# Optimization experiments

Measured on AMD Instinct MI355X. Metric: run time of the kernel, lower is better.

The kernel has to match this reference:

```python
import jax, jax.numpy as jnp
import numpy as np

N_NODES = 100000
N_EDGES = 1600000
IN_DIM = 128
HID = 128
OUT_DIM = 64
EPS = 1e-8


def setup_inputs() -> dict:
    key = jax.random.key(0)
    ks = jax.random.split(key, 10)
    x = jax.random.normal(ks[0], (N_NODES, IN_DIM), dtype=jnp.float32)
    edge_index = jax.random.randint(ks[1], (2, N_EDGES), 0, N_NODES, dtype=jnp.int64)
    edge_attr = jax.random.uniform(ks[2], (N_EDGES, 4), dtype=jnp.float32)
    s1 = 1.0 / np.sqrt(IN_DIM)
    s2 = 1.0 / np.sqrt(HID)
    sr = 1.0 / np.sqrt(2 * HID)
    W1 = jax.random.normal(ks[3], (HID, IN_DIM), dtype=jnp.float32) * s1
    b1 = jnp.zeros((HID,), dtype=jnp.float32)
    W2 = jax.random.normal(ks[4], (HID, HID), dtype=jnp.float32) * s2
    b2 = jnp.zeros((HID,), dtype=jnp.float32)
    Wr = jax.random.normal(ks[5], (OUT_DIM, 2 * HID), dtype=jnp.float32) * sr
    br = jnp.zeros((OUT_DIM,), dtype=jnp.float32)
    return {"x": x, "edge_index": edge_index, "edge_attr": edge_attr,
            "W1": W1, "b1": b1, "W2": W2, "b2": b2, "Wr": Wr, "br": br}


def _edge_weight_from_attr_auto(edge_attr):
    # mean over features, min-max normalize, invert, clamp >= 0
    m = edge_attr.mean(axis=-1)                      # [E]
    m_min, m_max = m.min(), m.max()
    m_norm = (m - m_min) / (m_max - m_min + EPS)
    w = jnp.where(m_max - m_min > EPS, 1.0 - m_norm, jnp.ones_like(m))
    return jnp.clip(w, 0.0)


def reference(x, edge_index, edge_attr, W1, b1, W2, b2, Wr, br):
    N = x.shape[0]
    row, col = edge_index[0], edge_index[1]          # source -> target
    ew = _edge_weight_from_attr_auto(edge_attr)      # [E]
    # GCN normalization with self-loops (self-loop weight = 1.0)
    deg = jax.ops.segment_sum(ew, col, num_segments=N) + 1.0   # [N]
    dis = jax.lax.rsqrt(deg)                         # deg >= 1
    norm = dis[row] * ew * dis[col]                  # [E]

    def gcn(h, W, b):
        hW = h @ W.T                                 # [N, d_out]
        agg = jax.ops.segment_sum(norm[:, None] * hW[row], col, num_segments=N)
        # self-loop contribution: dis[i] * 1.0 * dis[i] * hW[i]
        return agg + (dis * dis)[:, None] * hW + b

    # dropout in eval mode -> identity
    h1 = jax.nn.relu(gcn(x, W1, b1))                 # [N, HID]
    h2 = jax.nn.relu(gcn(h1, W2, b2))                # [N, HID]
    hcat = jnp.concatenate([h1, h2], axis=-1)        # [N, 2*HID] (JK concat)
    return hcat @ Wr.T + br                          # residue-level [N, OUT_DIM]
```

## Files before the change

kernel.cpp:

```cpp
#include <hip/hip_runtime.h>

#define NN 100000
#define NE 1600000
#define HID 128
#define ODIM 64
#define NBK 196
#define BSHIFT 9
#define BGRID 512
#define CVTB 48
#define CHUNK 3125
#define BITER 13
#define BINCAP 12288
#define SMAX 4504
#define LMAX 568

typedef unsigned int u32;
typedef unsigned short u16;
typedef __bf16 bf16x8 __attribute__((ext_vector_type(8)));
typedef float f32x4 __attribute__((ext_vector_type(4)));
typedef float f32x2 __attribute__((ext_vector_type(2)));

__device__ __forceinline__ float bf_lo(u32 p){ return __uint_as_float(p << 16); }
__device__ __forceinline__ float bf_hi(u32 p){ return __uint_as_float(p & 0xffff0000u); }
__device__ __forceinline__ u16 f2bf(float f){
  u32 u = __float_as_uint(f);
  u += 0x7fffu + ((u >> 16) & 1u);
  return (u16)(u >> 16);
}
__device__ __forceinline__ bf16x8 ld8bf(const u16* p){ return *(const bf16x8*)p; }
__device__ __forceinline__ bf16x8 cvt8(const float* p){
  union { bf16x8 v; u16 s[8]; } r;
#pragma unroll
  for (int i = 0; i < 8; i++) r.s[i] = f2bf(p[i]);
  return r.v;
}

__global__ __launch_bounds__(256) void k_bin(
    const float* __restrict__ eattr, const int* __restrict__ erow,
    const int* __restrict__ ecol, u32* __restrict__ bcur,
    uint2* __restrict__ bin, u32* __restrict__ minmax, u32* __restrict__ cnt,
    const float* __restrict__ W1, const float* __restrict__ W2,
    const float* __restrict__ Wr, u16* __restrict__ W1b,
    u16* __restrict__ W2b, u16* __restrict__ Wrb){
  int tid = threadIdx.x;
  if (blockIdx.x >= BGRID){
    int i = (blockIdx.x - BGRID) * 256 + tid;
    const float* src; u16* dst; int off;
    if (i < 4096){ src = W1; dst = W1b; off = i; }
    else if (i < 8192){ src = W2; dst = W2b; off = i - 4096; }
    else { src = Wr; dst = Wrb; off = i - 8192; }
    float4 v = ((const float4*)src)[off];
    uint2 o;
    o.x = (u32)f2bf(v.x) | ((u32)f2bf(v.y) << 16);
    o.y = (u32)f2bf(v.z) | ((u32)f2bf(v.w) << 16);
    ((uint2*)dst)[off] = o;
    return;
  }
  __shared__ u32 lcnt4[4 * NBK], wof4[4 * NBK];
  __shared__ u32 lofs[NBK], gb[NBK];
  __shared__ u32 scn[256];
  __shared__ u16 lmap[LMAX];
  __shared__ uint2 stage[SMAX];
  __shared__ u32 Tt;
  __shared__ float smin[4], smax[4];
  for (int t = tid; t < 4 * NBK; t += 256) lcnt4[t] = 0;
  __syncthreads();
  int base = blockIdx.x * CHUNK;
  int wid = tid >> 6, lane = tid & 63;
  float lmin = __uint_as_float(0x7f800000u), lmax = 0.f;
  u32 pk[BITER]; float mv[BITER]; u32 sv[BITER];
#pragma unroll
  for (int it = 0; it < BITER; it++){
    int idx = it * 256 + tid;
    u32 p = 0xFFFFFFFFu; float m = 0.f; u32 s = 0;
    if (idx < CHUNK){
      int e = base + idx;
      float4 a = ((const float4*)eattr)[e];
      m = 0.25f * (a.x + a.y + a.z + a.w);
      lmin = fminf(lmin, m); lmax = fmaxf(lmax, m);
      int c = ecol[e];
      s = (u32)erow[e]; if (s >= NN) s = 0;
      if ((u32)c < NN){
        u32 b = (u32)c >> BSHIFT;
        u32 r = atomicAdd(&lcnt4[wid * NBK + b], 1u);
        p = (b << 21) | (((u32)c & 511u) << 12) | r;
        atomicAdd(&cnt[c], 1u);
      }
    }
    pk[it] = p; mv[it] = m; sv[it] = s;
  }
  __syncthreads();
  u32 na = 0, n = 0;
  if (tid < NBK){
    u32 n0 = lcnt4[tid], n1 = lcnt4[NBK + tid];
    u32 n2 = lcnt4[2 * NBK + tid], n3 = lcnt4[3 * NBK + tid];
    n = n0 + n1 + n2 + n3;
    na = (n + 7u) & ~7u;
    wof4[tid] = 0; wof4[NBK + tid] = n0;
    wof4[2 * NBK + tid] = n0 + n1; wof4[3 * NBK + tid] = n0 + n1 + n2;
  }
  scn[tid] = na; __syncthreads();
  for (int s = 1; s < 256; s <<= 1){
    u32 t = (tid >= s) ? scn[tid - s] : 0;
    __syncthreads();
    scn[tid] += t;
    __syncthreads();
  }
  u32 ex = scn[tid] - na;
  if (tid < NBK){
    lofs[tid] = ex;
    u32 g = 0x80000000u;
    if (na){
      u32 gl = atomicAdd(&bcur[tid], na);
      if (gl + na <= BINCAP) g = (u32)tid * BINCAP + gl;
    }
    gb[tid] = g;
    for (u32 l = ex >> 3; l < (ex + na) >> 3; l++) lmap[l] = (u16)tid;
    uint2 sent; sent.x = 0xFFFFFFFFu; sent.y = 0u;
    for (u32 k = n; k < na; k++) stage[ex + k] = sent;
  }
  if (tid == 255) Tt = scn[255];
  __syncthreads();
#pragma unroll
  for (int it = 0; it < BITER; it++){
    u32 p = pk[it];
    if (p == 0xFFFFFFFFu) continue;
    u32 b = p >> 21;
    uint2 rec; rec.x = sv[it] | (((p >> 12) & 511u) << 17); rec.y = __float_as_uint(mv[it]);
    stage[lofs[b] + wof4[wid * NBK + b] + (p & 4095u)] = rec;
  }
  __syncthreads();
  u32 T = Tt;
  for (u32 i = tid; i < T; i += 256){
    u32 b = lmap[i >> 3];
    u32 g = gb[b];
    if (g != 0x80000000u) bin[g + (i - lofs[b])] = stage[i];
  }
  for (int off = 32; off; off >>= 1){
    lmin = fminf(lmin, __shfl_xor(lmin, off));
    lmax = fmaxf(lmax, __shfl_xor(lmax, off));
  }
  if (lane == 0){ smin[wid] = lmin; smax[wid] = lmax; }
  __syncthreads();
  if (tid == 0){
    float mn = fminf(fminf(smin[0], smin[1]), fminf(smin[2], smin[3]));
    float mx = fmaxf(fmaxf(smax[0], smax[1]), fmaxf(smax[2], smax[3]));
    atomicMax(&minmax[0], ~__float_as_uint(mn));
    atomicMax(&minmax[1], __float_as_uint(mx));
  }
}

__global__ __launch_bounds__(512) void k_scan(
    const u32* __restrict__ cnt, u32* __restrict__ meta, u32* __restrict__ cur){
  __shared__ u32 wtot[8];
  int b = blockIdx.x, tid = threadIdx.x;
  int wid = tid >> 6, lane = tid & 63;
  int node = (b << BSHIFT) + tid;
  u32 v = (node < NN) ? cnt[node] : 0u;
  u32 incl = v;
  for (int off = 1; off < 64; off <<= 1){
    u32 t = (u32)__shfl_up((int)incl, off);
    if (lane >= off) incl += t;
  }
  if (lane == 63) wtot[wid] = incl;
  __syncthreads();
  u32 pre = 0;
#pragma unroll
  for (int k = 0; k < 8; k++) pre += (k < wid) ? wtot[k] : 0u;
  u32 rs = (u32)(b * BINCAP) + pre + incl - v;
  if (node < NN){
    meta[node] = rs | (v << 22);
    cur[node] = rs;
  }
}

__global__ __launch_bounds__(1024) void k_scatter(
    const u32* __restrict__ bcur, const uint2* __restrict__ bin,
    const u32* __restrict__ minmax, const u32* __restrict__ cur,
    u32* __restrict__ csr, float* __restrict__ dis){
  __shared__ u32 curL[512], degL[512];
  int b = blockIdx.x, tid = threadIdx.x;
  int bb = b * BINCAP;
  int nrec = (int)min(bcur[b], (u32)BINCAP);
  if (tid < 512){
    int node = (b << BSHIFT) + tid;
    curL[tid] = (node < NN) ? cur[node] : 0u;
    degL[tid] = 0u;
  }
  __syncthreads();
  float mn  = __uint_as_float(~minmax[0]);
  float mx  = __uint_as_float(minmax[1]);
  float rng = mx - mn;
  bool flat = !(rng > 1e-8f);
  float inv = 1.f / (rng + 1e-8f);
  for (int i = tid; i < nrec; i += 1024){
    uint2 r = bin[bb + i];
    if (r.x == 0xFFFFFFFFu) continue;
    u32 d = (r.x >> 17) & 511u;
    float w = flat ? 1.f : fmaxf(1.f - (__uint_as_float(r.y) - mn) * inv, 0.f);
    u32 pos = atomicAdd(&curL[d], 1u);
    csr[pos] = (r.x & 0x1FFFFu) | ((u32)(w * 32767.f + 0.5f) << 17);
    atomicAdd(&degL[d], (u32)(w * 1048576.f + 0.5f));
  }
  __syncthreads();
  if (tid < 512){
    int node = (b << BSHIFT) + tid;
    if (node < NN) dis[node] = rsqrtf(1.f + (float)degL[tid] * (1.f / 1048576.f));
  }
}

template <bool A_F32>
__global__ __launch_bounds__(256) void k_gemm128(
    const void* __restrict__ Av, const u16* __restrict__ Bt,
    const float* __restrict__ dis, u16* __restrict__ G){
  int wave = threadIdx.x >> 6, lane = threadIdx.x & 63;
  int m0 = blockIdx.x * 32;
  int m = lane & 15, q = lane >> 4;
  const float* a0f = (const float*)Av + (size_t)(m0 + m) * HID;
  const float* a1f = a0f + (size_t)16 * HID;
  const u16*   a0b = (const u16*)Av   + (size_t)(m0 + m) * HID;
  const u16*   a1b = a0b + (size_t)16 * HID;
  const u16* brow0 = Bt + (size_t)(wave * 16 + m) * HID;
  const u16* brow1 = brow0 + (size_t)64 * HID;
  f32x4 acc00 = {0.f,0.f,0.f,0.f}, acc01 = {0.f,0.f,0.f,0.f};
  f32x4 acc10 = {0.f,0.f,0.f,0.f}, acc11 = {0.f,0.f,0.f,0.f};
#pragma unroll
  for (int kb = 0; kb < HID; kb += 32){
    bf16x8 af0 = A_F32 ? cvt8(a0f + kb + q * 8) : ld8bf(a0b + kb + q * 8);
    bf16x8 af1 = A_F32 ? cvt8(a1f + kb + q * 8) : ld8bf(a1b + kb + q * 8);
    bf16x8 bf0 = ld8bf(brow0 + kb + q * 8);
    bf16x8 bf1 = ld8bf(brow1 + kb + q * 8);
    acc00 = __builtin_amdgcn_mfma_f32_16x16x32_bf16(af0, bf0, acc00, 0, 0, 0);
    acc01 = __builtin_amdgcn_mfma_f32_16x16x32_bf16(af0, bf1, acc01, 0, 0, 0);
    acc10 = __builtin_amdgcn_mfma_f32_16x16x32_bf16(af1, bf0, acc10, 0, 0, 0);
    acc11 = __builtin_amdgcn_mfma_f32_16x16x32_bf16(af1, bf1, acc11, 0, 0, 0);
  }
  u16* crow0 = G + (size_t)(m0 + q * 4) * HID + wave * 16 + m;
  u16* crow1 = crow0 + (size_t)16 * HID;
#pragma unroll
  for (int r = 0; r < 4; r++){
    float d0 = dis[m0 + q * 4 + r];
    float d1 = dis[m0 + 16 + q * 4 + r];
    crow0[(size_t)r * HID]      = f2bf(acc00[r] * d0);
    crow0[(size_t)r * HID + 64] = f2bf(acc01[r] * d0);
    crow1[(size_t)r * HID]      = f2bf(acc10[r] * d1);
    crow1[(size_t)r * HID + 64] = f2bf(acc11[r] * d1);
  }
}

__global__ __launch_bounds__(256) void k_aggregate(
    const u32* __restrict__ meta, const u32* __restrict__ csr,
    const float* __restrict__ dis, const u16* __restrict__ g,
    const float* __restrict__ bias, u16* __restrict__ hout){
  int node = __builtin_amdgcn_readfirstlane(
      (int)(blockIdx.x * 4 + (threadIdx.x >> 6)));
  int lane = threadIdx.x & 63;
  const u32* gp = (const u32*)g;
  u32 sv = gp[((size_t)node << 6) + lane];
  u32 mw = meta[node];
  float di = dis[node];
  u32 s = mw & 0x3FFFFFu;
  int c = (int)(mw >> 22);
  const u32* cp = csr + s;
  f32x2 acc = {0.f, 0.f};
  int j = 0;
  for (; j + 16 <= c; j += 16){
    u32 p[16];
#pragma unroll
    for (int t = 0; t < 16; t++)
      p[t] = __builtin_amdgcn_readfirstlane(cp[j + t]);
    u32 pv[16];
#pragma unroll
    for (int t = 0; t < 16; t++)
      pv[t] = gp[(size_t)(p[t] & 0x1FFFFu) * 64u + lane];
#pragma unroll
    for (int t = 0; t < 16; t++){
      float wf = (float)(p[t] >> 17);
      f32x2 val = {bf_lo(pv[t]), bf_hi(pv[t])};
      f32x2 w2 = {wf, wf};
      acc += w2 * val;
    }
  }
  for (; j < c; j += 8){
    u32 p[8];
#pragma unroll
    for (int t = 0; t < 8; t++)
      p[t] = __builtin_amdgcn_readfirstlane(cp[j + t]);
    u32 st[8]; u32 wi[8];
#pragma unroll
    for (int t = 0; t < 8; t++){
      bool ok = (j + t) < c;
      st[t] = ok ? (p[t] & 0x1FFFFu) : 0u;
      wi[t] = ok ? (p[t] >> 17) : 0u;
    }
    u32 pv[8];
#pragma unroll
    for (int t = 0; t < 8; t++)
      pv[t] = gp[(size_t)st[t] * 64u + lane];
#pragma unroll
    for (int t = 0; t < 8; t++){
      float wf = (float)wi[t];
      f32x2 val = {bf_lo(pv[t]), bf_hi(pv[t])};
      f32x2 w2 = {wf, wf};
      acc += w2 * val;
    }
  }
  float2 bv = ((const float2*)bias)[lane];
  f32x2 selfv = {bf_lo(sv), bf_hi(sv)};
  float d2 = di * (1.f / 32767.f);
  float o0 = fmaxf(acc.x * d2 + (selfv.x * di + bv.x), 0.f);
  float o1 = fmaxf(acc.y * d2 + (selfv.y * di + bv.y), 0.f);
  ((u32*)hout)[((size_t)node << 6) + lane] = (u32)f2bf(o0) | ((u32)f2bf(o1) << 16);
}

__global__ __launch_bounds__(256) void k_readout(
    const u16* __restrict__ h1, const u16* __restrict__ h2,
    const u16* __restrict__ Wrb, const float* __restrict__ br, float* __restrict__ out){
  int wave = threadIdx.x >> 6, lane = threadIdx.x & 63;
  int m0 = blockIdx.x * 32;
  int n0 = wave * 16;
  int m = lane & 15, q = lane >> 4;
  const u16* a10 = h1 + (size_t)(m0 + m) * HID;
  const u16* a11 = a10 + (size_t)16 * HID;
  const u16* a20 = h2 + (size_t)(m0 + m) * HID;
  const u16* a21 = a20 + (size_t)16 * HID;
  const u16* b  = Wrb + (size_t)(n0 + m) * (2 * HID);
  f32x4 acc0 = {0.f,0.f,0.f,0.f}, acc1 = {0.f,0.f,0.f,0.f};
#pragma unroll
  for (int kb = 0; kb < HID; kb += 32){
    bf16x8 bf = ld8bf(b + kb + q * 8);
    acc0 = __builtin_amdgcn_mfma_f32_16x16x32_bf16(ld8bf(a10 + kb + q * 8), bf, acc0, 0, 0, 0);
    acc1 = __builtin_amdgcn_mfma_f32_16x16x32_bf16(ld8bf(a11 + kb + q * 8), bf, acc1, 0, 0, 0);
  }
#pragma unroll
  for (int kb = 0; kb < HID; kb += 32){
    bf16x8 bf = ld8bf(b + HID + kb + q * 8);
    acc0 = __builtin_amdgcn_mfma_f32_16x16x32_bf16(ld8bf(a20 + kb + q * 8), bf, acc0, 0, 0, 0);
    acc1 = __builtin_amdgcn_mfma_f32_16x16x32_bf16(ld8bf(a21 + kb + q * 8), bf, acc1, 0, 0, 0);
  }
  float bias = br[n0 + m];
  float* crow0 = out + (size_t)(m0 + q * 4) * ODIM + n0 + m;
  float* crow1 = crow0 + (size_t)16 * ODIM;
#pragma unroll
  for (int r = 0; r < 4; r++){
    crow0[(size_t)r * ODIM] = acc0[r] + bias;
    crow1[(size_t)r * ODIM] = acc1[r] + bias;
  }
}

extern "C" void kernel_launch(void* const* d_in, const int* in_sizes, int n_in,
                              void* d_out, int out_size, void* d_ws, size_t ws_size,
                              hipStream_t stream){
  const float* x     = (const float*)d_in[0];
  const int*   eidx  = (const int*)d_in[1];
  const float* eattr = (const float*)d_in[2];
  const float* W1    = (const float*)d_in[3];
  const float* b1    = (const float*)d_in[4];
  const float* W2    = (const float*)d_in[5];
  const float* b2    = (const float*)d_in[6];
  const float* Wr    = (const float*)d_in[7];
  const float* br    = (const float*)d_in[8];
  const int* erow  = eidx;
  const int* ecol  = eidx + NE;

  char* w = (char*)d_ws;
  auto carve = [&](size_t bytes) -> void* {
    void* p = (void*)w;
    w += (bytes + 255) & ~(size_t)255;
    return p;
  };
  u32* csr       = (u32*)carve((size_t)NBK * BINCAP * 4);
  u32* bcur      = (u32*)carve(256 * 4);
  u32* minmax    = (u32*)carve(256);
  u32* cnt       = (u32*)carve((size_t)NN * 4);
  u32* cur       = (u32*)carve((size_t)NN * 4);
  u32* meta      = (u32*)carve((size_t)NN * 4);
  float* dis     = (float*)carve((size_t)NN * 4);
  u16* W1b       = (u16*)carve((size_t)HID * HID * 2);
  u16* W2b       = (u16*)carve((size_t)HID * HID * 2);
  u16* Wrb       = (u16*)carve((size_t)ODIM * 2 * HID * 2);
  u16* g         = (u16*)carve((size_t)NN * HID * 2);
  u16* h1        = (u16*)carve((size_t)NN * HID * 2);
  u16* h2        = (u16*)carve((size_t)NN * HID * 2);
  uint2* bin     = (uint2*)h2;

  size_t zspan = (size_t)((char*)cnt + (size_t)NN * 4 - (char*)bcur);
  hipMemsetAsync(bcur, 0, zspan, stream);
  k_bin<<<BGRID + CVTB, 256, 0, stream>>>(eattr, erow, ecol, bcur, bin, minmax,
                                          cnt, W1, W2, Wr, W1b, W2b, Wrb);
  k_scan<<<NBK, 512, 0, stream>>>(cnt, meta, cur);
  k_scatter<<<NBK, 1024, 0, stream>>>(bcur, bin, minmax, cur, csr, dis);

  k_gemm128<true><<<NN / 32, 256, 0, stream>>>(x, W1b, dis, g);
  k_aggregate<<<NN / 4, 256, 0, stream>>>(meta, csr, dis, g, b1, h1);
  k_gemm128<false><<<NN / 32, 256, 0, stream>>>(h1, W2b, dis, g);
  k_aggregate<<<NN / 4, 256, 0, stream>>>(meta, csr, dis, g, b2, h2);
  k_readout<<<NN / 32, 256, 0, stream>>>(h1, h2, Wrb, br, (float*)d_out);
}
```

Measured before the change: 429.0 us.

## Quantize edge means, defer min-max normalization, and fuse degree scan into scatter

Edge attribute means are quantized to 15-bit integers in the binning pass, so min/max become integer atomics and the edge weight becomes an affine function of the stored code, applied later. The global per-node count atomics and the separate scan kernel are removed. Counts, weight sums, the per-bin prefix scan and dis are now computed inside the scatter kernel from the binned records. The bin record shrinks from 8 to 6 bytes, split into u32 and u16 arrays, and the binning grid is enlarged with smaller chunks. The risk is quantizing the mean before normalization, which changes accuracy slightly. The scatter kernel also gains an extra pass over the bin.

```diff
diff --git a/kernel.cpp b/kernel.cpp
--- a/kernel.cpp
+++ b/kernel.cpp
@@ -6,13 +6,13 @@
 #define ODIM 64
 #define NBK 196
 #define BSHIFT 9
-#define BGRID 512
+#define BGRID 800
 #define CVTB 48
-#define CHUNK 3125
-#define BITER 13
+#define CHUNK 2000
+#define BITER 8
 #define BINCAP 12288
-#define SMAX 4504
-#define LMAX 568
+#define SMAX 2588
+#define LMAX 647
 
 typedef unsigned int u32;
 typedef unsigned short u16;
@@ -35,10 +35,19 @@
   return r.v;
 }
 
+__device__ __forceinline__ void wparams(const u32* minmax, float* A, float* B){
+  u32 mnq = 32767u - minmax[0];
+  u32 mxq = minmax[1];
+  u32 rngq = mxq - mnq;
+  float inv = rngq ? 1.f / ((float)rngq * (1.f / 32767.f) + 1e-8f) : 0.f;
+  *A = 1.f + (float)mnq * (1.f / 32767.f) * inv;
+  *B = inv * (1.f / 32767.f);
+}
+
 __global__ __launch_bounds__(256) void k_bin(
     const float* __restrict__ eattr, const int* __restrict__ erow,
     const int* __restrict__ ecol, u32* __restrict__ bcur,
-    uint2* __restrict__ bin, u32* __restrict__ minmax, u32* __restrict__ cnt,
+    u32* __restrict__ binA, u16* __restrict__ binM, u32* __restrict__ minmax,
     const float* __restrict__ W1, const float* __restrict__ W2,
     const float* __restrict__ Wr, u16* __restrict__ W1b,
     u16* __restrict__ W2b, u16* __restrict__ Wrb){
@@ -60,34 +69,36 @@
   __shared__ u32 lofs[NBK], gb[NBK];
   __shared__ u32 scn[256];
   __shared__ u16 lmap[LMAX];
-  __shared__ uint2 stage[SMAX];
+  __shared__ u32 stageA[SMAX];
+  __shared__ u16 stageM[SMAX];
   __shared__ u32 Tt;
-  __shared__ float smin[4], smax[4];
+  __shared__ u32 sMn[4], sMx[4];
   for (int t = tid; t < 4 * NBK; t += 256) lcnt4[t] = 0;
   __syncthreads();
   int base = blockIdx.x * CHUNK;
   int wid = tid >> 6, lane = tid & 63;
-  float lmin = __uint_as_float(0x7f800000u), lmax = 0.f;
-  u32 pk[BITER]; float mv[BITER]; u32 sv[BITER];
+  u32 lmn = 0, lmx = 0;
+  u32 pk[BITER], sd[BITER], mq8[BITER];
 #pragma unroll
   for (int it = 0; it < BITER; it++){
     int idx = it * 256 + tid;
-    u32 p = 0xFFFFFFFFu; float m = 0.f; u32 s = 0;
+    u32 p = 0xFFFFFFFFu, srcd = 0, mq = 0;
     if (idx < CHUNK){
       int e = base + idx;
       float4 a = ((const float4*)eattr)[e];
-      m = 0.25f * (a.x + a.y + a.z + a.w);
-      lmin = fminf(lmin, m); lmax = fmaxf(lmax, m);
+      float m = 0.25f * (a.x + a.y + a.z + a.w);
+      mq = (u32)(m * 32767.f + 0.5f);
+      lmn = max(lmn, 32767u - mq); lmx = max(lmx, mq);
       int c = ecol[e];
-      s = (u32)erow[e]; if (s >= NN) s = 0;
+      u32 s = (u32)erow[e]; if (s >= NN) s = 0;
       if ((u32)c < NN){
         u32 b = (u32)c >> BSHIFT;
         u32 r = atomicAdd(&lcnt4[wid * NBK + b], 1u);
-        p = (b << 21) | (((u32)c & 511u) << 12) | r;
-        atomicAdd(&cnt[c], 1u);
+        p = (b << 21) | r;
+        srcd = s | (((u32)c & 511u) << 17);
       }
     }
-    pk[it] = p; mv[it] = m; sv[it] = s;
+    pk[it] = p; sd[it] = srcd; mq8[it] = mq;
   }
   __syncthreads();
   u32 na = 0, n = 0;
@@ -95,7 +106,7 @@
     u32 n0 = lcnt4[tid], n1 = lcnt4[NBK + tid];
     u32 n2 = lcnt4[2 * NBK + tid], n3 = lcnt4[3 * NBK + tid];
     n = n0 + n1 + n2 + n3;
-    na = (n + 7u) & ~7u;
+    na = (n + 3u) & ~3u;
     wof4[tid] = 0; wof4[NBK + tid] = n0;
     wof4[2 * NBK + tid] = n0 + n1; wof4[3 * NBK + tid] = n0 + n1 + n2;
   }
@@ -115,9 +126,8 @@
       if (gl + na <= BINCAP) g = (u32)tid * BINCAP + gl;
     }
     gb[tid] = g;
-    for (u32 l = ex >> 3; l < (ex + na) >> 3; l++) lmap[l] = (u16)tid;
-    uint2 sent; sent.x = 0xFFFFFFFFu; sent.y = 0u;
-    for (u32 k = n; k < na; k++) stage[ex + k] = sent;
+    for (u32 l = ex >> 2; l < (ex + na) >> 2; l++) lmap[l] = (u16)tid;
+    for (u32 k = n; k < na; k++){ stageA[ex + k] = 0xFFFFFFFFu; stageM[ex + k] = 0; }
   }
   if (tid == 255) Tt = scn[255];
   __syncthreads();
@@ -126,86 +136,86 @@
     u32 p = pk[it];
     if (p == 0xFFFFFFFFu) continue;
     u32 b = p >> 21;
-    uint2 rec; rec.x = sv[it] | (((p >> 12) & 511u) << 17); rec.y = __float_as_uint(mv[it]);
-    stage[lofs[b] + wof4[wid * NBK + b] + (p & 4095u)] = rec;
+    u32 slot = lofs[b] + wof4[wid * NBK + b] + (p & 4095u);
+    stageA[slot] = sd[it];
+    stageM[slot] = (u16)mq8[it];
   }
   __syncthreads();
   u32 T = Tt;
   for (u32 i = tid; i < T; i += 256){
-    u32 b = lmap[i >> 3];
+    u32 b = lmap[i >> 2];
     u32 g = gb[b];
-    if (g != 0x80000000u) bin[g + (i - lofs[b])] = stage[i];
+    if (g != 0x80000000u){
+      u32 o = g + (i - lofs[b]);
+      binA[o] = stageA[i];
+      binM[o] = stageM[i];
+    }
   }
   for (int off = 32; off; off >>= 1){
-    lmin = fminf(lmin, __shfl_xor(lmin, off));
-    lmax = fmaxf(lmax, __shfl_xor(lmax, off));
-  }
-  if (lane == 0){ smin[wid] = lmin; smax[wid] = lmax; }
+    lmn = max(lmn, (u32)__shfl_xor((int)lmn, off));
+    lmx = max(lmx, (u32)__shfl_xor((int)lmx, off));
+  }
+  if (lane == 0){ sMn[wid] = lmn; sMx[wid] = lmx; }
   __syncthreads();
   if (tid == 0){
-    float mn = fminf(fminf(smin[0], smin[1]), fminf(smin[2], smin[3]));
-    float mx = fmaxf(fmaxf(smax[0], smax[1]), fmaxf(smax[2], smax[3]));
-    atomicMax(&minmax[0], ~__float_as_uint(mn));
-    atomicMax(&minmax[1], __float_as_uint(mx));
-  }
-}
-
-__global__ __launch_bounds__(512) void k_scan(
-    const u32* __restrict__ cnt, u32* __restrict__ meta, u32* __restrict__ cur){
+    u32 mn = max(max(sMn[0], sMn[1]), max(sMn[2], sMn[3]));
+    u32 mx = max(max(sMx[0], sMx[1]), max(sMx[2], sMx[3]));
+    atomicMax(&minmax[0], mn);
+    atomicMax(&minmax[1], mx);
+  }
+}
+
+__global__ __launch_bounds__(1024) void k_scatter(
+    const u32* __restrict__ bcur, const u32* __restrict__ binA,
+    const u16* __restrict__ binM, const u32* __restrict__ minmax,
+    u32* __restrict__ csr, u32* __restrict__ meta, float* __restrict__ dis){
+  __shared__ u32 cntL[512], sumL[512], curL[512];
   __shared__ u32 wtot[8];
   int b = blockIdx.x, tid = threadIdx.x;
+  int bb = b * BINCAP;
+  int nrec = (int)min(bcur[b], (u32)BINCAP);
+  if (tid < 512){ cntL[tid] = 0; sumL[tid] = 0; }
+  __syncthreads();
+  for (int i = tid; i < nrec; i += 1024){
+    u32 a = binA[bb + i];
+    if (a == 0xFFFFFFFFu) continue;
+    u32 d = (a >> 17) & 511u;
+    u32 mq = binM[bb + i];
+    atomicAdd(&cntL[d], 1u);
+    atomicAdd(&sumL[d], mq);
+  }
+  __syncthreads();
+  float A, B; wparams(minmax, &A, &B);
   int wid = tid >> 6, lane = tid & 63;
-  int node = (b << BSHIFT) + tid;
-  u32 v = (node < NN) ? cnt[node] : 0u;
-  u32 incl = v;
+  u32 v = 0, incl = 0;
+  if (tid < 512){ v = cntL[tid]; incl = v; }
   for (int off = 1; off < 64; off <<= 1){
     u32 t = (u32)__shfl_up((int)incl, off);
     if (lane >= off) incl += t;
   }
-  if (lane == 63) wtot[wid] = incl;
-  __syncthreads();
-  u32 pre = 0;
-#pragma unroll
-  for (int k = 0; k < 8; k++) pre += (k < wid) ? wtot[k] : 0u;
-  u32 rs = (u32)(b * BINCAP) + pre + incl - v;
-  if (node < NN){
-    meta[node] = rs | (v << 22);
-    cur[node] = rs;
-  }
-}
-
-__global__ __launch_bounds__(1024) void k_scatter(
-    const u32* __restrict__ bcur, const uint2* __restrict__ bin,
-    const u32* __restrict__ minmax, const u32* __restrict__ cur,
-    u32* __restrict__ csr, float* __restrict__ dis){
-  __shared__ u32 curL[512], degL[512];
-  int b = blockIdx.x, tid = threadIdx.x;
-  int bb = b * BINCAP;
-  int nrec = (int)min(bcur[b], (u32)BINCAP);
+  if (tid < 512 && lane == 63) wtot[wid] = incl;
+  __syncthreads();
   if (tid < 512){
+    u32 pre = 0;
+#pragma unroll
+    for (int k = 0; k < 8; k++) pre += (k < wid) ? wtot[k] : 0u;
+    u32 ex = pre + incl - v;
+    curL[tid] = (u32)bb + ex;
     int node = (b << BSHIFT) + tid;
-    curL[tid] = (node < NN) ? cur[node] : 0u;
-    degL[tid] = 0u;
-  }
-  __syncthreads();
-  float mn  = __uint_as_float(~minmax[0]);
-  float mx  = __uint_as_float(minmax[1]);
-  float rng = mx - mn;
-  bool flat = !(rng > 1e-8f);
-  float inv = 1.f / (rng + 1e-8f);
+    if (node < NN){
+      meta[node] = ((u32)bb + ex) | (v << 22);
+      float sw = A * (float)v - B * (float)sumL[tid];
+      dis[node] = rsqrtf(1.f + sw);
+    }
+  }
+  __syncthreads();
   for (int i = tid; i < nrec; i += 1024){
-    uint2 r = bin[bb + i];
-    if (r.x == 0xFFFFFFFFu) continue;
-    u32 d = (r.x >> 17) & 511u;
-    float w = flat ? 1.f : fmaxf(1.f - (__uint_as_float(r.y) - mn) * inv, 0.f);
+    u32 a = binA[bb + i];
+    if (a == 0xFFFFFFFFu) continue;
+    u32 d = (a >> 17) & 511u;
+    u32 mq = binM[bb + i];
     u32 pos = atomicAdd(&curL[d], 1u);
-    csr[pos] = (r.x & 0x1FFFFu) | ((u32)(w * 32767.f + 0.5f) << 17);
-    atomicAdd(&degL[d], (u32)(w * 1048576.f + 0.5f));
-  }
-  __syncthreads();
-  if (tid < 512){
-    int node = (b << BSHIFT) + tid;
-    if (node < NN) dis[node] = rsqrtf(1.f + (float)degL[tid] * (1.f / 1048576.f));
+    csr[pos] = (a & 0x1FFFFu) | (mq << 17);
   }
 }
 
@@ -250,8 +260,9 @@
 
 __global__ __launch_bounds__(256) void k_aggregate(
     const u32* __restrict__ meta, const u32* __restrict__ csr,
-    const float* __restrict__ dis, const u16* __restrict__ g,
-    const float* __restrict__ bias, u16* __restrict__ hout){
+    const float* __restrict__ dis, const u32* __restrict__ minmax,
+    const u16* __restrict__ g, const float* __restrict__ bias,
+    u16* __restrict__ hout){
   int node = __builtin_amdgcn_readfirstlane(
       (int)(blockIdx.x * 4 + (threadIdx.x >> 6)));
   int lane = threadIdx.x & 63;
@@ -259,6 +270,7 @@
   u32 sv = gp[((size_t)node << 6) + lane];
   u32 mw = meta[node];
   float di = dis[node];
+  float A, B; wparams(minmax, &A, &B);
   u32 s = mw & 0x3FFFFFu;
   int c = (int)(mw >> 22);
   const u32* cp = csr + s;
@@ -275,7 +287,7 @@
       pv[t] = gp[(size_t)(p[t] & 0x1FFFFu) * 64u + lane];
 #pragma unroll
     for (int t = 0; t < 16; t++){
-      float wf = (float)(p[t] >> 17);
+      float wf = A - B * (float)(p[t] >> 17);
       f32x2 val = {bf_lo(pv[t]), bf_hi(pv[t])};
       f32x2 w2 = {wf, wf};
       acc += w2 * val;
@@ -286,12 +298,12 @@
 #pragma unroll
     for (int t = 0; t < 8; t++)
       p[t] = __builtin_amdgcn_readfirstlane(cp[j + t]);
-    u32 st[8]; u32 wi[8];
+    u32 st[8]; float wv[8];
 #pragma unroll
     for (int t = 0; t < 8; t++){
       bool ok = (j + t) < c;
       st[t] = ok ? (p[t] & 0x1FFFFu) : 0u;
-      wi[t] = ok ? (p[t] >> 17) : 0u;
+      wv[t] = ok ? (A - B * (float)(p[t] >> 17)) : 0.f;
     }
     u32 pv[8];
 #pragma unroll
@@ -299,17 +311,15 @@
       pv[t] = gp[(size_t)st[t] * 64u + lane];
 #pragma unroll
     for (int t = 0; t < 8; t++){
-      float wf = (float)wi[t];
       f32x2 val = {bf_lo(pv[t]), bf_hi(pv[t])};
-      f32x2 w2 = {wf, wf};
+      f32x2 w2 = {wv[t], wv[t]};
       acc += w2 * val;
     }
   }
   float2 bv = ((const float2*)bias)[lane];
   f32x2 selfv = {bf_lo(sv), bf_hi(sv)};
-  float d2 = di * (1.f / 32767.f);
-  float o0 = fmaxf(acc.x * d2 + (selfv.x * di + bv.x), 0.f);
-  float o1 = fmaxf(acc.y * d2 + (selfv.y * di + bv.y), 0.f);
+  float o0 = fmaxf((acc.x + selfv.x) * di + bv.x, 0.f);
+  float o1 = fmaxf((acc.y + selfv.y) * di + bv.y, 0.f);
   ((u32*)hout)[((size_t)node << 6) + lane] = (u32)f2bf(o0) | ((u32)f2bf(o1) << 16);
 }
 
@@ -370,10 +380,8 @@
     return p;
   };
   u32* csr       = (u32*)carve((size_t)NBK * BINCAP * 4);
-  u32* bcur      = (u32*)carve(256 * 4);
+  u32* bcur      = (u32*)carve(1024);
   u32* minmax    = (u32*)carve(256);
-  u32* cnt       = (u32*)carve((size_t)NN * 4);
-  u32* cur       = (u32*)carve((size_t)NN * 4);
   u32* meta      = (u32*)carve((size_t)NN * 4);
   float* dis     = (float*)carve((size_t)NN * 4);
   u16* W1b       = (u16*)carve((size_t)HID * HID * 2);
@@ -382,18 +390,17 @@
   u16* g         = (u16*)carve((size_t)NN * HID * 2);
   u16* h1        = (u16*)carve((size_t)NN * HID * 2);
   u16* h2        = (u16*)carve((size_t)NN * HID * 2);
-  uint2* bin     = (uint2*)h2;
-
-  size_t zspan = (size_t)((char*)cnt + (size_t)NN * 4 - (char*)bcur);
-  hipMemsetAsync(bcur, 0, zspan, stream);
-  k_bin<<<BGRID + CVTB, 256, 0, stream>>>(eattr, erow, ecol, bcur, bin, minmax,
-                                          cnt, W1, W2, Wr, W1b, W2b, Wrb);
-  k_scan<<<NBK, 512, 0, stream>>>(cnt, meta, cur);
-  k_scatter<<<NBK, 1024, 0, stream>>>(bcur, bin, minmax, cur, csr, dis);
+  u32* binA      = (u32*)h2;
+  u16* binM      = (u16*)((char*)h2 + (size_t)NBK * BINCAP * 4);
+
+  hipMemsetAsync(bcur, 0, 1280, stream);
+  k_bin<<<BGRID + CVTB, 256, 0, stream>>>(eattr, erow, ecol, bcur, binA, binM,
+                                          minmax, W1, W2, Wr, W1b, W2b, Wrb);
+  k_scatter<<<NBK, 1024, 0, stream>>>(bcur, binA, binM, minmax, csr, meta, dis);
 
   k_gemm128<true><<<NN / 32, 256, 0, stream>>>(x, W1b, dis, g);
-  k_aggregate<<<NN / 4, 256, 0, stream>>>(meta, csr, dis, g, b1, h1);
+  k_aggregate<<<NN / 4, 256, 0, stream>>>(meta, csr, dis, minmax, g, b1, h1);
   k_gemm128<false><<<NN / 32, 256, 0, stream>>>(h1, W2b, dis, g);
-  k_aggregate<<<NN / 4, 256, 0, stream>>>(meta, csr, dis, g, b2, h2);
+  k_aggregate<<<NN / 4, 256, 0, stream>>>(meta, csr, dis, minmax, g, b2, h2);
   k_readout<<<NN / 32, 256, 0, stream>>>(h1, h2, Wrb, br, (float*)d_out);
 }
```

Result: faster. 397.4 us (-7.4%).
